# Kernel optimization log

Hardware: AMD Instinct MI355X
Metric: run time of the kernel (lower is better)

The kernel has to match this reference:

```python
import jax, jax.numpy as jnp
import numpy as np

HEAD_DIM = 64
NUM_HEADS = 32
ROPE_BASE = 10000.0


def _rope_interleaved(x):
    # x: [B, T, H, D]; interleaved RoPE on query, seqlen_offset = 0
    B, T, H, D = x.shape
    inv_freq = 1.0 / (ROPE_BASE ** (jnp.arange(0, D, 2, dtype=jnp.float32) / D))  # [D/2]
    t = jnp.arange(T, dtype=jnp.float32)
    freqs = t[:, None] * inv_freq[None, :]          # [T, D/2]
    cos = jnp.cos(freqs)[None, :, None, :]          # [1, T, 1, D/2]
    sin = jnp.sin(freqs)[None, :, None, :]
    x1 = x[..., 0::2]
    x2 = x[..., 1::2]
    o1 = x1 * cos - x2 * sin
    o2 = x1 * sin + x2 * cos
    out = jnp.stack([o1, o2], axis=-1).reshape(x.shape)  # re-interleave
    return out


def setup_inputs() -> dict:
    key = jax.random.key(0)
    k1, k2, k3, k4, k5 = jax.random.split(key, 5)
    B, T, Dm = 2, 2048, 2048
    H, Dh = NUM_HEADS, HEAD_DIM
    scale = 0.02
    return {
        "hidden_states": jax.random.normal(k1, (B, T, Dm), jnp.float32),
        "shared_k": jax.random.normal(k2, (B, T, H, Dh), jnp.float32),
        "shared_v": jax.random.normal(k3, (B, T, H, Dh), jnp.float32),
        "Wq": jax.random.normal(k4, (Dm, Dm), jnp.float32) * scale,
        "Wo": jax.random.normal(k5, (Dm, Dm), jnp.float32) * scale,
    }


def reference(hidden_states, shared_k, shared_v, Wq, Wo):
    B, T, Dm = hidden_states.shape
    H, Dh = NUM_HEADS, HEAD_DIM
    # q projection (nn.Linear: x @ W.T)
    q = (hidden_states @ Wq.T).reshape(B, T, H, Dh)
    # rotary on q only (seqlen_offset = shared_k_len - q_len = 0)
    q = _rope_interleaved(q)
    # parallel causal attention over shared KV cache (window_size=None)
    scale = 1.0 / jnp.sqrt(jnp.asarray(Dh, jnp.float32))
    scores = jnp.einsum('bqhd,bkhd->bhqk', q, shared_k) * scale
    causal = jnp.tril(jnp.ones((T, T), dtype=bool))
    scores = jnp.where(causal[None, None], scores, -jnp.inf)
    p = jax.nn.softmax(scores, axis=-1)
    o = jnp.einsum('bhqk,bkhd->bqhd', p, shared_v)
    o = o.reshape(B, T, Dm)
    return o @ Wo.T
```

## Files before the change

kernel.cpp:

```cpp
#include <hip/hip_runtime.h>
#include <stdint.h>

typedef short short8 __attribute__((ext_vector_type(8)));
typedef float f32x4 __attribute__((ext_vector_type(4)));

#define QSCALE 0.1803368801111137f
#define FREQC 0.4152410118609203f

__device__ __forceinline__ float bf2f(unsigned short u) {
    union { unsigned int i; float f; } x; x.i = ((unsigned int)u) << 16; return x.f;
}
__device__ __forceinline__ unsigned short f2bf(float f) {
    union { float f; unsigned int i; } x; x.f = f;
    unsigned int i = x.i;
    unsigned int r = i + 0x7FFFu + ((i >> 16) & 1u);
    return (unsigned short)(r >> 16);
}

#define GLDS16(g, l) \
    __builtin_amdgcn_global_load_lds((const __attribute__((address_space(1))) void*)(g), \
                                     (__attribute__((address_space(3))) void*)(l), 16, 0, 0)

__global__ void cvt_all(const float* __restrict__ hs, const float* __restrict__ k,
                        const float* __restrict__ wq, const float* __restrict__ wo,
                        unsigned short* __restrict__ hs_b, unsigned short* __restrict__ k_b,
                        unsigned short* __restrict__ wq_b, unsigned short* __restrict__ wo_b) {
    int blk = blockIdx.x;
    const float* in; unsigned short* out; int i;
    if (blk < 8192)        { in = hs; out = hs_b; i = blk * 256 + threadIdx.x; }
    else if (blk < 16384)  { in = k;  out = k_b;  i = (blk - 8192) * 256 + threadIdx.x; }
    else if (blk < 20480)  { in = wq; out = wq_b; i = (blk - 16384) * 256 + threadIdx.x; }
    else                   { in = wo; out = wo_b; i = (blk - 20480) * 256 + threadIdx.x; }
    float4 v = ((const float4*)in)[i];
    ushort4 o;
    o.x = f2bf(v.x); o.y = f2bf(v.y); o.z = f2bf(v.z); o.w = f2bf(v.w);
    ((ushort4*)out)[i] = o;
}

__global__ __launch_bounds__(256) void transpose_v(const float* __restrict__ V, unsigned short* __restrict__ Vt) {
    __shared__ float s[64 * 65];
    int t0 = blockIdx.x * 64;
    int bh = blockIdx.y;
    int b = bh >> 5, h = bh & 31;
    int tid = threadIdx.x;
#pragma unroll
    for (int it = 0; it < 4; ++it) {
        int c = tid + it * 256;
        int t = c >> 4;
        int d0 = (c & 15) * 4;
        float4 v = *(const float4*)(V + (size_t)(((b * 2048 + t0 + t) * 32 + h)) * 64 + d0);
        s[t * 65 + d0 + 0] = v.x; s[t * 65 + d0 + 1] = v.y;
        s[t * 65 + d0 + 2] = v.z; s[t * 65 + d0 + 3] = v.w;
    }
    __syncthreads();
#pragma unroll
    for (int it = 0; it < 2; ++it) {
        int c = tid + it * 256;
        int d = c >> 3;
        int tt = (c & 7) * 8;
        short8 pk;
#pragma unroll
        for (int j = 0; j < 8; ++j) pk[j] = (short)f2bf(s[(tt + j) * 65 + d]);
        *(short8*)(Vt + (size_t)(bh * 64 + d) * 2048 + t0 + tt) = pk;
    }
}

template <bool BF16_OUT>
__global__ __launch_bounds__(256) void gemm_bt(
    const unsigned short* __restrict__ A,
    const unsigned short* __restrict__ B,
    void* __restrict__ Cout,
    int M, int N, int K)
{
    __shared__ __align__(16) unsigned short lA[128 * 64];
    __shared__ __align__(16) unsigned short lB[128 * 64];
    int tid = threadIdx.x, lane = tid & 63, wave = tid >> 6;
    int wm = (wave >> 1) * 64, wn = (wave & 1) * 64;
    int m16 = lane & 15, q = lane >> 4;
    int rowBase = blockIdx.x * 128, colBase = blockIdx.y * 128;
    f32x4 acc[4][4] = {};

    int sr = lane >> 3;
    int g  = (lane & 7) ^ sr;
    const unsigned short* gAp = A + (size_t)(rowBase + wave * 32 + sr) * K + g * 8;
    const unsigned short* gBp = B + (size_t)(colBase + wave * 32 + sr) * K + g * 8;
    unsigned short* lAd = &lA[(wave * 32) * 64];
    unsigned short* lBd = &lB[(wave * 32) * 64];

    for (int k0 = 0; k0 < K; k0 += 64) {
        __syncthreads();
#pragma unroll
        for (int i = 0; i < 4; ++i) {
            GLDS16(gAp + (size_t)(8 * i) * K + k0, lAd + (8 * i) * 64);
            GLDS16(gBp + (size_t)(8 * i) * K + k0, lBd + (8 * i) * 64);
        }
        __syncthreads();
#pragma unroll
        for (int kk = 0; kk < 2; ++kk) {
            short8 af[4], bfr[4];
#pragma unroll
            for (int i = 0; i < 4; ++i) {
                int RA = wm + i * 16 + m16;
                af[i]  = *(const short8*)&lA[RA * 64 + (((kk * 4 + q) ^ (RA & 7)) * 8)];
                int RB = wn + i * 16 + m16;
                bfr[i] = *(const short8*)&lB[RB * 64 + (((kk * 4 + q) ^ (RB & 7)) * 8)];
            }
#pragma unroll
            for (int i = 0; i < 4; ++i)
#pragma unroll
                for (int jn = 0; jn < 4; ++jn)
                    acc[i][jn] = __builtin_amdgcn_mfma_f32_16x16x32_bf16(af[i], bfr[jn], acc[i][jn], 0, 0, 0);
        }
    }
#pragma unroll
    for (int i = 0; i < 4; ++i)
#pragma unroll
        for (int jn = 0; jn < 4; ++jn)
#pragma unroll
            for (int r = 0; r < 4; ++r) {
                int row = rowBase + wm + i * 16 + q * 4 + r;
                int col = colBase + wn + jn * 16 + m16;
                float v = acc[i][jn][r];
                if (BF16_OUT) ((unsigned short*)Cout)[(size_t)row * N + col] = f2bf(v);
                else          ((float*)Cout)[(size_t)row * N + col] = v;
            }
}

#define PROCESS(AQ0, AQ1, LRUN, ACCO, QT)                                          \
    do {                                                                           \
        bool diag = (kt == (QT));                                                  \
        _Pragma("unroll")                                                          \
        for (int nt = 0; nt < 4; ++nt) {                                           \
            f32x4 z = {0.f, 0.f, 0.f, 0.f};                                        \
            short8 bk0 = *(const short8*)&sK[(nt * 16 + m16) * SL + q * 8];        \
            short8 bk1 = *(const short8*)&sK[(nt * 16 + m16) * SL + 32 + q * 8];   \
            z = __builtin_amdgcn_mfma_f32_16x16x32_bf16(AQ0, bk0, z, 0, 0, 0);     \
            z = __builtin_amdgcn_mfma_f32_16x16x32_bf16(AQ1, bk1, z, 0, 0, 0);     \
            _Pragma("unroll")                                                      \
            for (int r = 0; r < 4; ++r) {                                          \
                float s = z[r];                                                    \
                if (diag) {                                                        \
                    int key = nt * 16 + m16;                                       \
                    int qi = w * 16 + q * 4 + r;                                   \
                    if (key > qi) s = -__builtin_inff();                           \
                }                                                                  \
                float pv = __builtin_amdgcn_exp2f(s);                              \
                LRUN[r] += pv;                                                     \
                sP[w][(q * 4 + r) * SL + nt * 16 + m16] = f2bf(pv);                \
            }                                                                      \
        }                                                                          \
        short8 ap0 = *(const short8*)&sP[w][m16 * SL + q * 8];                     \
        short8 ap1 = *(const short8*)&sP[w][m16 * SL + 32 + q * 8];                \
        _Pragma("unroll")                                                          \
        for (int nt = 0; nt < 4; ++nt) {                                           \
            short8 bv0 = *(const short8*)&sV[(nt * 16 + m16) * SL + q * 8];        \
            short8 bv1 = *(const short8*)&sV[(nt * 16 + m16) * SL + 32 + q * 8];   \
            ACCO[nt] = __builtin_amdgcn_mfma_f32_16x16x32_bf16(ap0, bv0, ACCO[nt], 0, 0, 0); \
            ACCO[nt] = __builtin_amdgcn_mfma_f32_16x16x32_bf16(ap1, bv1, ACCO[nt], 0, 0, 0); \
        }                                                                          \
    } while (0)

__global__ __launch_bounds__(256, 3) void attn(
    const unsigned short* __restrict__ Q,
    const unsigned short* __restrict__ Kb,
    const unsigned short* __restrict__ Vt,
    unsigned short* __restrict__ O)
{
    const int SL = 72;
    __shared__ __align__(16) unsigned short sK[64 * SL];
    __shared__ __align__(16) unsigned short sV[64 * SL];
    __shared__ __align__(16) unsigned short sP[4][16 * SL];
    int tid = threadIdx.x, lane = tid & 63, w = tid >> 6;
    int m16 = lane & 15, q = lane >> 4;
    int flat = blockIdx.x;
    int bh = flat & 63, p = flat >> 6;
    int b = bh >> 5, h = bh & 31;
    int qtA = 31 - p, qtB = p;

    short8 aqA0, aqA1, aqB0, aqB1;
    {
        int tA = qtA * 64 + w * 16 + m16;
        int tB = qtB * 64 + w * 16 + m16;
        const unsigned short* rowA = Q + (size_t)(b * 2048 + tA) * 2048 + h * 64 + q * 8;
        const unsigned short* rowB = Q + (size_t)(b * 2048 + tB) * 2048 + h * 64 + q * 8;
        short8 a0 = *(const short8*)rowA, a1 = *(const short8*)(rowA + 32);
        short8 b0 = *(const short8*)rowB, b1 = *(const short8*)(rowB + 32);
        float tfA = (float)tA, tfB = (float)tB;
#pragma unroll
        for (int j = 0; j < 4; ++j) {
            float inv0 = __builtin_amdgcn_exp2f(-FREQC * (float)(q * 4 + j));
            float inv1 = __builtin_amdgcn_exp2f(-FREQC * (float)(16 + q * 4 + j));
            float cA0 = __cosf(tfA * inv0), sA0 = __sinf(tfA * inv0);
            float cA1 = __cosf(tfA * inv1), sA1 = __sinf(tfA * inv1);
            float cB0 = __cosf(tfB * inv0), sB0 = __sinf(tfB * inv0);
            float cB1 = __cosf(tfB * inv1), sB1 = __sinf(tfB * inv1);
            float x1, x2;
            x1 = bf2f((unsigned short)a0[2 * j]); x2 = bf2f((unsigned short)a0[2 * j + 1]);
            aqA0[2 * j]     = (short)f2bf((x1 * cA0 - x2 * sA0) * QSCALE);
            aqA0[2 * j + 1] = (short)f2bf((x1 * sA0 + x2 * cA0) * QSCALE);
            x1 = bf2f((unsigned short)a1[2 * j]); x2 = bf2f((unsigned short)a1[2 * j + 1]);
            aqA1[2 * j]     = (short)f2bf((x1 * cA1 - x2 * sA1) * QSCALE);
            aqA1[2 * j + 1] = (short)f2bf((x1 * sA1 + x2 * cA1) * QSCALE);
            x1 = bf2f((unsigned short)b0[2 * j]); x2 = bf2f((unsigned short)b0[2 * j + 1]);
            aqB0[2 * j]     = (short)f2bf((x1 * cB0 - x2 * sB0) * QSCALE);
            aqB0[2 * j + 1] = (short)f2bf((x1 * sB0 + x2 * cB0) * QSCALE);
            x1 = bf2f((unsigned short)b1[2 * j]); x2 = bf2f((unsigned short)b1[2 * j + 1]);
            aqB1[2 * j]     = (short)f2bf((x1 * cB1 - x2 * sB1) * QSCALE);
            aqB1[2 * j + 1] = (short)f2bf((x1 * sB1 + x2 * cB1) * QSCALE);
        }
    }

    float lrunA[4] = {0.f, 0.f, 0.f, 0.f}, lrunB[4] = {0.f, 0.f, 0.f, 0.f};
    f32x4 accOA[4], accOB[4];
#pragma unroll
    for (int nt = 0; nt < 4; ++nt) {
        f32x4 z = {0.f, 0.f, 0.f, 0.f};
        accOA[nt] = z; accOB[nt] = z;
    }

    int cK = tid >> 3, c8 = tid & 7;
    const unsigned short* kbase = Kb + (size_t)(b * 2048) * 2048 + h * 64;
    const unsigned short* vbase = Vt + (size_t)((b * 32 + h) * 64) * 2048;

    for (int kt = 0; kt <= qtA; ++kt) {
        int kBase = kt * 64;
        __syncthreads();
#pragma unroll
        for (int it = 0; it < 2; ++it) {
            int row = cK + it * 32;
            *(float4*)&sK[row * SL + c8 * 8] =
                *(const float4*)(kbase + (size_t)(kBase + row) * 2048 + c8 * 8);
            *(float4*)&sV[row * SL + c8 * 8] =
                *(const float4*)(vbase + (size_t)row * 2048 + kBase + c8 * 8);
        }
        __syncthreads();

        PROCESS(aqA0, aqA1, lrunA, accOA, qtA);
        if (kt <= qtB) PROCESS(aqB0, aqB1, lrunB, accOB, qtB);
    }

#pragma unroll
    for (int r = 0; r < 4; ++r) {
        float la = lrunA[r], lb = lrunB[r];
        la += __shfl_xor(la, 1); lb += __shfl_xor(lb, 1);
        la += __shfl_xor(la, 2); lb += __shfl_xor(lb, 2);
        la += __shfl_xor(la, 4); lb += __shfl_xor(lb, 4);
        la += __shfl_xor(la, 8); lb += __shfl_xor(lb, 8);
        lrunA[r] = 1.0f / la; lrunB[r] = 1.0f / lb;
    }
#pragma unroll
    for (int nt = 0; nt < 4; ++nt)
#pragma unroll
        for (int r = 0; r < 4; ++r) {
            int col = h * 64 + nt * 16 + m16;
            O[(size_t)(b * 2048 + qtA * 64 + w * 16 + q * 4 + r) * 2048 + col] =
                f2bf(accOA[nt][r] * lrunA[r]);
            O[(size_t)(b * 2048 + qtB * 64 + w * 16 + q * 4 + r) * 2048 + col] =
                f2bf(accOB[nt][r] * lrunB[r]);
        }
}

extern "C" void kernel_launch(void* const* d_in, const int* in_sizes, int n_in,
                              void* d_out, int out_size, void* d_ws, size_t ws_size,
                              hipStream_t stream) {
    const float* hs = (const float*)d_in[0];
    const float* sk = (const float*)d_in[1];
    const float* sv = (const float*)d_in[2];
    const float* wq = (const float*)d_in[3];
    const float* wo = (const float*)d_in[4];
    float* out = (float*)d_out;

    char* ws = (char*)d_ws;
    unsigned short* hid_b = (unsigned short*)(ws);
    unsigned short* wq_b  = (unsigned short*)(ws + ((size_t)16 << 20));
    unsigned short* wo_b  = (unsigned short*)(ws + ((size_t)24 << 20));
    unsigned short* k_b   = (unsigned short*)(ws + ((size_t)32 << 20));
    unsigned short* vt_b  = (unsigned short*)(ws + ((size_t)48 << 20));
    unsigned short* q_b   = (unsigned short*)(ws + ((size_t)64 << 20));
    unsigned short* o_b   = (unsigned short*)(ws + ((size_t)80 << 20));

    cvt_all<<<24576, 256, 0, stream>>>(hs, sk, wq, wo, hid_b, k_b, wq_b, wo_b);
    transpose_v<<<dim3(32, 64), 256, 0, stream>>>(sv, vt_b);
    gemm_bt<true><<<dim3(32, 16), 256, 0, stream>>>(hid_b, wq_b, (void*)q_b, 4096, 2048, 2048);
    attn<<<1024, 256, 0, stream>>>(q_b, k_b, vt_b, o_b);
    gemm_bt<false><<<dim3(32, 16), 256, 0, stream>>>(o_b, wo_b, (void*)out, 4096, 2048, 2048);
}
```

Measured before the change: 329.2 us.

## Double-buffer GEMM and attention LDS tiles; keep P in registers via transposed QK

The GEMM gets two LDS buffers with async global_load_lds prefetch of the next K tile while the current one is computed, so one barrier per iteration replaces two. The attention kernel likewise double-buffers swizzled K/V tiles loaded asynchronously. It computes S^T (K as the A operand) so the exp'd probabilities can be packed with v_cvt_pk_bf16 directly into the PV MFMA operand, removing the sP shared-memory round trip. Occupancy hint rises to 4 blocks per SM. The risks are register pressure and the correctness of the new operand layouts.

After: 287.4 us. 12.7% less time.

```diff
diff --git a/kernel.cpp b/kernel.cpp
--- a/kernel.cpp
+++ b/kernel.cpp
@@ -3,6 +3,8 @@
 
 typedef short short8 __attribute__((ext_vector_type(8)));
 typedef float f32x4 __attribute__((ext_vector_type(4)));
+typedef int int2v __attribute__((ext_vector_type(2)));
+typedef int int4v __attribute__((ext_vector_type(4)));
 
 #define QSCALE 0.1803368801111137f
 #define FREQC 0.4152410118609203f
@@ -15,6 +17,11 @@
     unsigned int i = x.i;
     unsigned int r = i + 0x7FFFu + ((i >> 16) & 1u);
     return (unsigned short)(r >> 16);
+}
+__device__ __forceinline__ int cvtpk_bf16(float lo, float hi) {
+    int r;
+    asm("v_cvt_pk_bf16_f32 %0, %1, %2" : "=v"(r) : "v"(lo), "v"(hi));
+    return r;
 }
 
 #define GLDS16(g, l) \
@@ -72,8 +79,8 @@
     void* __restrict__ Cout,
     int M, int N, int K)
 {
-    __shared__ __align__(16) unsigned short lA[128 * 64];
-    __shared__ __align__(16) unsigned short lB[128 * 64];
+    __shared__ __align__(16) unsigned short lA[2][128 * 64];
+    __shared__ __align__(16) unsigned short lB[2][128 * 64];
     int tid = threadIdx.x, lane = tid & 63, wave = tid >> 6;
     int wm = (wave >> 1) * 64, wn = (wave & 1) * 64;
     int m16 = lane & 15, q = lane >> 4;
@@ -84,26 +91,32 @@
     int g  = (lane & 7) ^ sr;
     const unsigned short* gAp = A + (size_t)(rowBase + wave * 32 + sr) * K + g * 8;
     const unsigned short* gBp = B + (size_t)(colBase + wave * 32 + sr) * K + g * 8;
-    unsigned short* lAd = &lA[(wave * 32) * 64];
-    unsigned short* lBd = &lB[(wave * 32) * 64];
-
+
+#define GSTAGE(buf, k0)                                                                   \
+    do {                                                                                  \
+        _Pragma("unroll")                                                                 \
+        for (int i = 0; i < 4; ++i) {                                                     \
+            GLDS16(gAp + (size_t)(8 * i) * K + (k0), &lA[buf][(wave * 32 + 8 * i) * 64]); \
+            GLDS16(gBp + (size_t)(8 * i) * K + (k0), &lB[buf][(wave * 32 + 8 * i) * 64]); \
+        }                                                                                 \
+    } while (0)
+
+    GSTAGE(0, 0);
+    __syncthreads();
+    int cur = 0;
     for (int k0 = 0; k0 < K; k0 += 64) {
-        __syncthreads();
-#pragma unroll
-        for (int i = 0; i < 4; ++i) {
-            GLDS16(gAp + (size_t)(8 * i) * K + k0, lAd + (8 * i) * 64);
-            GLDS16(gBp + (size_t)(8 * i) * K + k0, lBd + (8 * i) * 64);
-        }
-        __syncthreads();
+        if (k0 + 64 < K) GSTAGE(cur ^ 1, k0 + 64);
+        const unsigned short* la = lA[cur];
+        const unsigned short* lb = lB[cur];
 #pragma unroll
         for (int kk = 0; kk < 2; ++kk) {
             short8 af[4], bfr[4];
 #pragma unroll
             for (int i = 0; i < 4; ++i) {
                 int RA = wm + i * 16 + m16;
-                af[i]  = *(const short8*)&lA[RA * 64 + (((kk * 4 + q) ^ (RA & 7)) * 8)];
+                af[i]  = *(const short8*)&la[RA * 64 + (((kk * 4 + q) ^ (RA & 7)) * 8)];
                 int RB = wn + i * 16 + m16;
-                bfr[i] = *(const short8*)&lB[RB * 64 + (((kk * 4 + q) ^ (RB & 7)) * 8)];
+                bfr[i] = *(const short8*)&lb[RB * 64 + (((kk * 4 + q) ^ (RB & 7)) * 8)];
             }
 #pragma unroll
             for (int i = 0; i < 4; ++i)
@@ -111,6 +124,8 @@
                 for (int jn = 0; jn < 4; ++jn)
                     acc[i][jn] = __builtin_amdgcn_mfma_f32_16x16x32_bf16(af[i], bfr[jn], acc[i][jn], 0, 0, 0);
         }
+        __syncthreads();
+        cur ^= 1;
     }
 #pragma unroll
     for (int i = 0; i < 4; ++i)
@@ -126,52 +141,17 @@
             }
 }
 
-#define PROCESS(AQ0, AQ1, LRUN, ACCO, QT)                                          \
-    do {                                                                           \
-        bool diag = (kt == (QT));                                                  \
-        _Pragma("unroll")                                                          \
-        for (int nt = 0; nt < 4; ++nt) {                                           \
-            f32x4 z = {0.f, 0.f, 0.f, 0.f};                                        \
-            short8 bk0 = *(const short8*)&sK[(nt * 16 + m16) * SL + q * 8];        \
-            short8 bk1 = *(const short8*)&sK[(nt * 16 + m16) * SL + 32 + q * 8];   \
-            z = __builtin_amdgcn_mfma_f32_16x16x32_bf16(AQ0, bk0, z, 0, 0, 0);     \
-            z = __builtin_amdgcn_mfma_f32_16x16x32_bf16(AQ1, bk1, z, 0, 0, 0);     \
-            _Pragma("unroll")                                                      \
-            for (int r = 0; r < 4; ++r) {                                          \
-                float s = z[r];                                                    \
-                if (diag) {                                                        \
-                    int key = nt * 16 + m16;                                       \
-                    int qi = w * 16 + q * 4 + r;                                   \
-                    if (key > qi) s = -__builtin_inff();                           \
-                }                                                                  \
-                float pv = __builtin_amdgcn_exp2f(s);                              \
-                LRUN[r] += pv;                                                     \
-                sP[w][(q * 4 + r) * SL + nt * 16 + m16] = f2bf(pv);                \
-            }                                                                      \
-        }                                                                          \
-        short8 ap0 = *(const short8*)&sP[w][m16 * SL + q * 8];                     \
-        short8 ap1 = *(const short8*)&sP[w][m16 * SL + 32 + q * 8];                \
-        _Pragma("unroll")                                                          \
-        for (int nt = 0; nt < 4; ++nt) {                                           \
-            short8 bv0 = *(const short8*)&sV[(nt * 16 + m16) * SL + q * 8];        \
-            short8 bv1 = *(const short8*)&sV[(nt * 16 + m16) * SL + 32 + q * 8];   \
-            ACCO[nt] = __builtin_amdgcn_mfma_f32_16x16x32_bf16(ap0, bv0, ACCO[nt], 0, 0, 0); \
-            ACCO[nt] = __builtin_amdgcn_mfma_f32_16x16x32_bf16(ap1, bv1, ACCO[nt], 0, 0, 0); \
-        }                                                                          \
-    } while (0)
-
-__global__ __launch_bounds__(256, 3) void attn(
+__global__ __launch_bounds__(256, 4) void attn(
     const unsigned short* __restrict__ Q,
     const unsigned short* __restrict__ Kb,
     const unsigned short* __restrict__ Vt,
     unsigned short* __restrict__ O)
 {
-    const int SL = 72;
-    __shared__ __align__(16) unsigned short sK[64 * SL];
-    __shared__ __align__(16) unsigned short sV[64 * SL];
-    __shared__ __align__(16) unsigned short sP[4][16 * SL];
+    __shared__ __align__(16) unsigned short sK[2][64 * 64];
+    __shared__ __align__(16) unsigned short sV[2][64 * 64];
     int tid = threadIdx.x, lane = tid & 63, w = tid >> 6;
     int m16 = lane & 15, q = lane >> 4;
+    int rx = m16 & 7;
     int flat = blockIdx.x;
     int bh = flat & 63, p = flat >> 6;
     int b = bh >> 5, h = bh & 31;
@@ -210,7 +190,7 @@
         }
     }
 
-    float lrunA[4] = {0.f, 0.f, 0.f, 0.f}, lrunB[4] = {0.f, 0.f, 0.f, 0.f};
+    float lrunA = 0.f, lrunB = 0.f;
     f32x4 accOA[4], accOB[4];
 #pragma unroll
     for (int nt = 0; nt < 4; ++nt) {
@@ -218,35 +198,109 @@
         accOA[nt] = z; accOB[nt] = z;
     }
 
-    int cK = tid >> 3, c8 = tid & 7;
-    const unsigned short* kbase = Kb + (size_t)(b * 2048) * 2048 + h * 64;
-    const unsigned short* vbase = Vt + (size_t)((b * 32 + h) * 64) * 2048;
-
+    int sr = lane >> 3, g = (lane & 7) ^ sr;
+    int rb = w * 16;
+    const unsigned short* kgp = Kb + (size_t)(b * 2048 + rb + sr) * 2048 + h * 64 + g * 8;
+    const unsigned short* vgp = Vt + (size_t)((b * 32 + h) * 64 + rb + sr) * 2048 + g * 8;
+
+#define ASTAGE(kt, bi)                                                              \
+    do {                                                                            \
+        int kb0 = (kt) * 64;                                                        \
+        _Pragma("unroll")                                                           \
+        for (int i = 0; i < 2; ++i) {                                               \
+            GLDS16(kgp + (size_t)(kb0 + 8 * i) * 2048, &sK[bi][(rb + 8 * i) * 64]); \
+            GLDS16(vgp + (size_t)(8 * i) * 2048 + kb0, &sV[bi][(rb + 8 * i) * 64]); \
+        }                                                                           \
+    } while (0)
+
+    ASTAGE(0, 0);
+    __syncthreads();
+    int cur = 0;
     for (int kt = 0; kt <= qtA; ++kt) {
-        int kBase = kt * 64;
+        if (kt < qtA) ASTAGE(kt + 1, cur ^ 1);
+        bool doB = (kt <= qtB);
+        bool diagA = (kt == qtA), diagB = (kt == qtB);
+        const unsigned short* kbuf = sK[cur];
+        const unsigned short* vbuf = sV[cur];
+
+        int pkA[4][2], pkB[4][2];
+#pragma unroll
+        for (int nt = 0; nt < 4; ++nt) {
+            const unsigned short* kr = kbuf + (nt * 16 + m16) * 64;
+            short8 bk0 = *(const short8*)&kr[(q ^ rx) * 8];
+            short8 bk1 = *(const short8*)&kr[((4 + q) ^ rx) * 8];
+            f32x4 zA = {0.f, 0.f, 0.f, 0.f};
+            zA = __builtin_amdgcn_mfma_f32_16x16x32_bf16(bk0, aqA0, zA, 0, 0, 0);
+            zA = __builtin_amdgcn_mfma_f32_16x16x32_bf16(bk1, aqA1, zA, 0, 0, 0);
+            float e[4];
+#pragma unroll
+            for (int r = 0; r < 4; ++r) {
+                float s = zA[r];
+                if (diagA && (nt * 16 + q * 4 + r > w * 16 + m16)) s = -__builtin_inff();
+                e[r] = __builtin_amdgcn_exp2f(s);
+            }
+            lrunA += (e[0] + e[1]) + (e[2] + e[3]);
+            pkA[nt][0] = cvtpk_bf16(e[0], e[1]);
+            pkA[nt][1] = cvtpk_bf16(e[2], e[3]);
+            if (doB) {
+                f32x4 zB = {0.f, 0.f, 0.f, 0.f};
+                zB = __builtin_amdgcn_mfma_f32_16x16x32_bf16(bk0, aqB0, zB, 0, 0, 0);
+                zB = __builtin_amdgcn_mfma_f32_16x16x32_bf16(bk1, aqB1, zB, 0, 0, 0);
+                float eb[4];
+#pragma unroll
+                for (int r = 0; r < 4; ++r) {
+                    float s = zB[r];
+                    if (diagB && (nt * 16 + q * 4 + r > w * 16 + m16)) s = -__builtin_inff();
+                    eb[r] = __builtin_amdgcn_exp2f(s);
+                }
+                lrunB += (eb[0] + eb[1]) + (eb[2] + eb[3]);
+                pkB[nt][0] = cvtpk_bf16(eb[0], eb[1]);
+                pkB[nt][1] = cvtpk_bf16(eb[2], eb[3]);
+            }
+        }
+
+        int4v tA0 = {pkA[0][0], pkA[0][1], pkA[1][0], pkA[1][1]};
+        int4v tA1 = {pkA[2][0], pkA[2][1], pkA[3][0], pkA[3][1]};
+        short8 apA0 = __builtin_bit_cast(short8, tA0);
+        short8 apA1 = __builtin_bit_cast(short8, tA1);
+        short8 apB0, apB1;
+        if (doB) {
+            int4v tB0 = {pkB[0][0], pkB[0][1], pkB[1][0], pkB[1][1]};
+            int4v tB1 = {pkB[2][0], pkB[2][1], pkB[3][0], pkB[3][1]};
+            apB0 = __builtin_bit_cast(short8, tB0);
+            apB1 = __builtin_bit_cast(short8, tB1);
+        }
+
+#pragma unroll
+        for (int nt = 0; nt < 4; ++nt) {
+            const unsigned short* vr = vbuf + (nt * 16 + m16) * 64;
+            int2v a0 = *(const int2v*)&vr[(((q >> 1) + 0) ^ rx) * 8 + (q & 1) * 4];
+            int2v a1 = *(const int2v*)&vr[(((q >> 1) + 2) ^ rx) * 8 + (q & 1) * 4];
+            int2v a2 = *(const int2v*)&vr[(((q >> 1) + 4) ^ rx) * 8 + (q & 1) * 4];
+            int2v a3 = *(const int2v*)&vr[(((q >> 1) + 6) ^ rx) * 8 + (q & 1) * 4];
+            int4v tv0 = {a0.x, a0.y, a1.x, a1.y};
+            int4v tv1 = {a2.x, a2.y, a3.x, a3.y};
+            short8 bv0 = __builtin_bit_cast(short8, tv0);
+            short8 bv1 = __builtin_bit_cast(short8, tv1);
+            accOA[nt] = __builtin_amdgcn_mfma_f32_16x16x32_bf16(apA0, bv0, accOA[nt], 0, 0, 0);
+            accOA[nt] = __builtin_amdgcn_mfma_f32_16x16x32_bf16(apA1, bv1, accOA[nt], 0, 0, 0);
+            if (doB) {
+                accOB[nt] = __builtin_amdgcn_mfma_f32_16x16x32_bf16(apB0, bv0, accOB[nt], 0, 0, 0);
+                accOB[nt] = __builtin_amdgcn_mfma_f32_16x16x32_bf16(apB1, bv1, accOB[nt], 0, 0, 0);
+            }
+        }
         __syncthreads();
-#pragma unroll
-        for (int it = 0; it < 2; ++it) {
-            int row = cK + it * 32;
-            *(float4*)&sK[row * SL + c8 * 8] =
-                *(const float4*)(kbase + (size_t)(kBase + row) * 2048 + c8 * 8);
-            *(float4*)&sV[row * SL + c8 * 8] =
-                *(const float4*)(vbase + (size_t)row * 2048 + kBase + c8 * 8);
-        }
-        __syncthreads();
-
-        PROCESS(aqA0, aqA1, lrunA, accOA, qtA);
-        if (kt <= qtB) PROCESS(aqB0, aqB1, lrunB, accOB, qtB);
-    }
-
+        cur ^= 1;
+    }
+
+    lrunA += __shfl_xor(lrunA, 16); lrunA += __shfl_xor(lrunA, 32);
+    lrunB += __shfl_xor(lrunB, 16); lrunB += __shfl_xor(lrunB, 32);
+    float invA = 1.0f / lrunA, invB = 1.0f / lrunB;
+    float nA[4], nB[4];
 #pragma unroll
     for (int r = 0; r < 4; ++r) {
-        float la = lrunA[r], lb = lrunB[r];
-        la += __shfl_xor(la, 1); lb += __shfl_xor(lb, 1);
-        la += __shfl_xor(la, 2); lb += __shfl_xor(lb, 2);
-        la += __shfl_xor(la, 4); lb += __shfl_xor(lb, 4);
-        la += __shfl_xor(la, 8); lb += __shfl_xor(lb, 8);
-        lrunA[r] = 1.0f / la; lrunB[r] = 1.0f / lb;
+        nA[r] = __shfl(invA, q * 4 + r);
+        nB[r] = __shfl(invB, q * 4 + r);
     }
 #pragma unroll
     for (int nt = 0; nt < 4; ++nt)
@@ -254,9 +308,9 @@
         for (int r = 0; r < 4; ++r) {
             int col = h * 64 + nt * 16 + m16;
             O[(size_t)(b * 2048 + qtA * 64 + w * 16 + q * 4 + r) * 2048 + col] =
-                f2bf(accOA[nt][r] * lrunA[r]);
+                f2bf(accOA[nt][r] * nA[r]);
             O[(size_t)(b * 2048 + qtB * 64 + w * 16 + q * 4 + r) * 2048 + col] =
-                f2bf(accOB[nt][r] * lrunB[r]);
+                f2bf(accOB[nt][r] * nB[r]);
         }
 }
 
```
